# Optimization experiments

Hardware: AMD Instinct MI355X
Metric: run time of the kernel (lower is better)

Reference implementation:

```python
import jax, jax.numpy as jnp
import numpy as np
from jax import lax

C = 128
N_HEADS = 4
HEAD_D = C // N_HEADS
EXP = 2  # FFN expansion


def _ln_c(x, g, b, eps):
    # LayerNorm over channel dim of NCHW (equivalent to to_3d -> LN(c) -> to_4d)
    m = jnp.mean(x, axis=1, keepdims=True)
    v = jnp.mean((x - m) ** 2, axis=1, keepdims=True)
    return (x - m) / jnp.sqrt(v + eps) * g[None, :, None, None] + b[None, :, None, None]


def _conv1x1(x, w, b):
    # w: (out, in)
    return jnp.einsum('bchw,oc->bohw', x, w) + b[None, :, None, None]


def _dwconv(x, w, b):
    # depthwise conv, w: (Cg, 1, k, k), stride 1, SAME padding
    y = lax.conv_general_dilated(
        x, w, window_strides=(1, 1), padding='SAME',
        dimension_numbers=('NCHW', 'OIHW', 'NCHW'),
        feature_group_count=x.shape[1])
    return y + b[None, :, None, None]


def setup_inputs() -> dict:
    key = jax.random.key(0)
    ks = jax.random.split(key, 24)
    s = 0.05
    hid = C
    e = EXP * C
    inp = {
        'feats1': jax.random.normal(ks[0], (2, C, 64, 256), jnp.float32),
        'feats2': jax.random.normal(ks[1], (2, C, 64, 256), jnp.float32),
        # attention norms
        'an_g': jnp.ones((C,), jnp.float32), 'an_b': jnp.zeros((C,), jnp.float32),
        'anc_g': jnp.ones((C,), jnp.float32), 'anc_b': jnp.zeros((C,), jnp.float32),
        # qkv / out 1x1 convs
        'wq': jax.random.normal(ks[2], (hid, C), jnp.float32) * s,
        'bq': jnp.zeros((hid,), jnp.float32),
        'wkv': jax.random.normal(ks[3], (2 * hid, C), jnp.float32) * s,
        'bkv': jnp.zeros((2 * hid,), jnp.float32),
        'wo': jax.random.normal(ks[4], (C, hid), jnp.float32) * s,
        'bo': jnp.zeros((C,), jnp.float32),
        # FFN
        'fn_g': jnp.ones((C,), jnp.float32), 'fn_b': jnp.zeros((C,), jnp.float32),
        'w_in': jax.random.normal(ks[5], (e, C), jnp.float32) * s,
        'b_in': jnp.zeros((e,), jnp.float32),
        'w_dw3': jax.random.normal(ks[6], (e, 1, 3, 3), jnp.float32) * s,
        'b_dw3': jnp.zeros((e,), jnp.float32),
        'w_dw5': jax.random.normal(ks[7], (e, 1, 5, 5), jnp.float32) * s,
        'b_dw5': jnp.zeros((e,), jnp.float32),
        'w_dw7': jax.random.normal(ks[8], (e, 1, 7, 7), jnp.float32) * s,
        'b_dw7': jnp.zeros((e,), jnp.float32),
        'w_pw': jax.random.normal(ks[9], (e, 3 * e), jnp.float32) * s,
        'b_pw': jnp.zeros((e,), jnp.float32),
        'w_out': jax.random.normal(ks[10], (C, e), jnp.float32) * s,
        'b_out': jnp.zeros((C,), jnp.float32),
    }
    return inp


def reference(feats1, feats2, an_g, an_b, anc_g, anc_b, wq, bq, wkv, bkv, wo, bo,
              fn_g, fn_b, w_in, b_in, w_dw3, b_dw3, w_dw5, b_dw5, w_dw7, b_dw7,
              w_pw, b_pw, w_out, b_out):
    eps = 1e-6
    hid = C
    n, d = N_HEADS, HEAD_D
    scale = d ** (-0.5)

    # bi-directional cross attention: doubled batch
    cat1 = jnp.concatenate([feats1, feats2], axis=0)  # (B, C, H, W)
    cat2 = jnp.concatenate([feats2, feats1], axis=0)
    B, _, H, W = cat1.shape

    # pre-norm (separate norms for query and context streams)
    x1 = _ln_c(cat1, an_g, an_b, eps)
    x2 = _ln_c(cat2, anc_g, anc_b, eps)

    q = _conv1x1(x1, wq, bq)                     # (B, hid, H, W)
    kv = _conv1x1(x2, wkv, bkv)
    k, v = kv[:, :hid], kv[:, hid:]

    qh = q.reshape(B, n, d, H, W)
    kh = k.reshape(B, n, d, H, W)
    vh = v.reshape(B, n, d, H, W)

    # per-row (epipolar) attention over width
    sim = jnp.einsum('bndhi,bndhj->bnhij', qh, kh) * scale  # (B, n, H, W, W)
    # sink competition renorm
    attn = jax.nn.softmax(sim, axis=-1) + eps
    attn = attn / jnp.sum(attn, axis=-1, keepdims=True)

    o = jnp.einsum('bnhij,bndhj->bndhi', attn, vh).reshape(B, hid, H, W)
    o = _conv1x1(o, wo, bo)
    cat1 = cat1 + o

    # multiscale depthwise-conv FFN (receptive_aug='conv')
    y = _ln_c(cat1, fn_g, fn_b, 1e-5)
    y = jax.nn.silu(_conv1x1(y, w_in, b_in))     # (B, 2C, H, W)
    f3 = _dwconv(y, w_dw3, b_dw3)
    f5 = _dwconv(y, w_dw5, b_dw5)
    f7 = _dwconv(y, w_dw7, b_dw7)
    y = y + jax.nn.silu(_conv1x1(jnp.concatenate([f3, f5, f7], axis=1), w_pw, b_pw))
    y = _conv1x1(y, w_out, b_out)
    cat1 = cat1 + y

    half = B // 2
    return cat1[:half], cat1[half:]
```

## Files before the change

### kernel.cpp

```cpp
#include <hip/hip_runtime.h>

typedef unsigned short u16;
typedef unsigned int u32;

constexpr int H_ = 64;
constexpr int W_ = 256;
constexpr int HW_ = H_ * W_;

typedef __bf16 bf16x8 __attribute__((ext_vector_type(8)));
typedef float f32x4 __attribute__((ext_vector_type(4)));

__device__ __forceinline__ float bf2f(u16 v) { return __uint_as_float(((u32)v) << 16); }
__device__ __forceinline__ u16 f2bf(float f) {
  u32 x = __float_as_uint(f);
  u32 r = (x + 0x7fffu + ((x >> 16) & 1u)) >> 16;
  return (u16)r;
}
__device__ __forceinline__ float lo2f(u32 p) { return __uint_as_float(p << 16); }
__device__ __forceinline__ float hi2f(u32 p) { return __uint_as_float(p & 0xffff0000u); }
__device__ __forceinline__ void unpack8(uint4 v, float* f) {
  f[0] = lo2f(v.x); f[1] = hi2f(v.x);
  f[2] = lo2f(v.y); f[3] = hi2f(v.y);
  f[4] = lo2f(v.z); f[5] = hi2f(v.z);
  f[6] = lo2f(v.w); f[7] = hi2f(v.w);
}
__device__ __forceinline__ bf16x8 as_bf16x8(uint4 v) {
  union { uint4 u; bf16x8 b; } x; x.u = v; return x.b;
}
__device__ __forceinline__ int swz(int p, int c) { return c ^ (((p >> 3) & 3) << 3); }

constexpr int NT = 26;
constexpr int ELEMS_PER_BLK = 4096;
struct CvtArgs {
  const void* src[NT];
  u32 dst_off[NT];
  u32 n[NT];
  u32 blk_start[NT];
};

__global__ void convert_all(CvtArgs a, u16* __restrict__ dst) {
  const u32 bid = blockIdx.x;
  int ti = 0;
#pragma unroll
  for (int k = 1; k < NT; ++k) if (a.blk_start[k] <= bid) ti = k;
  const u32 e0 = (bid - a.blk_start[ti]) * ELEMS_PER_BLK;
  const u32 n = a.n[ti];
  u32 hi = e0 + ELEMS_PER_BLK; if (hi > n) hi = n;
  const float* sp = (const float*)a.src[ti];
  u16* d = dst + a.dst_off[ti];
  for (u32 i = e0 + threadIdx.x; i < hi; i += 256) d[i] = f2bf(sp[i]);
}

template <int CIN, int COUT>
__launch_bounds__(256)
__global__ void gemm1x1_ln(const u16* __restrict__ xA, const u16* __restrict__ xB,
                           const u16* __restrict__ w, const u16* __restrict__ bias,
                           const u16* __restrict__ lng, const u16* __restrict__ lnb,
                           float lneps, u16* __restrict__ out) {
  constexpr int POS = 64;
  constexpr int PITCH = CIN + 8;
  constexpr int MT = COUT / 64;
  __shared__ __align__(16) u16 xs[POS * PITCH];
  __shared__ float red1[256], red2[256], stm[64], str[64];
  const int t = threadIdx.x;
  const int b = blockIdx.y;
  const int pos0 = blockIdx.x * POS;

  const u16* basep = (b >= 2) ? xB : xA;
  const int bb = (b < 2) ? b : b - 2;
  const u16* xb16 = basep + (size_t)bb * CIN * HW_;

  constexpr int NLOAD = CIN * POS / 8;
  for (int idx = t; idx < NLOAD; idx += 256) {
    const int c = idx / (POS / 8);
    const int p8 = (idx % (POS / 8)) * 8;
    uint4 v = *(const uint4*)(xb16 + (size_t)c * HW_ + pos0 + p8);
    const int csw = swz(p8, c);
    u16* row = xs + p8 * PITCH + csw;
    row[0]         = (u16)v.x; row[PITCH]     = (u16)(v.x >> 16);
    row[2 * PITCH] = (u16)v.y; row[3 * PITCH] = (u16)(v.y >> 16);
    row[4 * PITCH] = (u16)v.z; row[5 * PITCH] = (u16)(v.z >> 16);
    row[6 * PITCH] = (u16)v.w; row[7 * PITCH] = (u16)(v.w >> 16);
  }
  __syncthreads();

  {
    const int p = t & 63, part = t >> 6;
    const int xorp = ((p >> 3) & 3) << 3;
    float s = 0.f, sq = 0.f;
#pragma unroll
    for (int k = 0; k < 32; k += 8) {
      uint4 v = *(const uint4*)(xs + p * PITCH + ((part * 32 + k) ^ xorp));
      float f[8]; unpack8(v, f);
#pragma unroll
      for (int j = 0; j < 8; ++j) { s += f[j]; sq += f[j] * f[j]; }
    }
    red1[part * 64 + p] = s; red2[part * 64 + p] = sq;
    __syncthreads();
    if (t < 64) {
      float ss = red1[t] + red1[64 + t] + red1[128 + t] + red1[192 + t];
      float qq = red2[t] + red2[64 + t] + red2[128 + t] + red2[192 + t];
      float m = ss * (1.0f / CIN);
      float var = qq * (1.0f / CIN) - m * m;
      var = var < 0.f ? 0.f : var;
      stm[t] = m; str[t] = rsqrtf(var + lneps);
    }
    __syncthreads();
    const float m = stm[p], r = str[p];
#pragma unroll
    for (int k = 0; k < 32; k += 8) {
      const int c = part * 32 + k;
      uint4 v = *(const uint4*)(xs + p * PITCH + (c ^ xorp));
      float f[8]; unpack8(v, f);
      u32 pk[4];
#pragma unroll
      for (int j = 0; j < 8; j += 2) {
        float g0 = bf2f(lng[c + j]), be0 = bf2f(lnb[c + j]);
        float g1 = bf2f(lng[c + j + 1]), be1 = bf2f(lnb[c + j + 1]);
        u16 lo = f2bf((f[j] - m) * r * g0 + be0);
        u16 hi = f2bf((f[j + 1] - m) * r * g1 + be1);
        pk[j >> 1] = (u32)lo | ((u32)hi << 16);
      }
      uint4 ov; ov.x = pk[0]; ov.y = pk[1]; ov.z = pk[2]; ov.w = pk[3];
      *(uint4*)(xs + p * PITCH + (c ^ xorp)) = ov;
    }
    __syncthreads();
  }

  const int lane = t & 63, wv = t >> 6;
  const int lo16 = lane & 15, quad = lane >> 4;
  const int orow0 = wv * MT * 16;
  const int qrow = quad * 4;

  f32x4 acc[MT][4];
#pragma unroll
  for (int mt = 0; mt < MT; ++mt) {
#pragma unroll
    for (int r = 0; r < 4; ++r) {
      const float bv = bf2f(bias[orow0 + mt * 16 + qrow + r]);
#pragma unroll
      for (int nt = 0; nt < 4; ++nt) acc[mt][nt][r] = bv;
    }
  }

  const u16* xb[4];
#pragma unroll
  for (int nt = 0; nt < 4; ++nt) {
    const int row = nt * 16 + lo16;
    xb[nt] = xs + row * PITCH + (quad * 8 ^ ((((row >> 3) & 3)) << 3));
  }
  const u16* wl = w + (size_t)(orow0 + lo16) * CIN + quad * 8;

#pragma unroll 2
  for (int kc = 0; kc < CIN / 32; ++kc) {
    const int c0 = kc * 32;
    bf16x8 bfr[4];
#pragma unroll
    for (int nt = 0; nt < 4; ++nt)
      bfr[nt] = as_bf16x8(*(const uint4*)(xb[nt] + c0));
#pragma unroll
    for (int mt = 0; mt < MT; ++mt) {
      bf16x8 afr = as_bf16x8(*(const uint4*)(wl + (size_t)mt * 16 * CIN + c0));
#pragma unroll
      for (int nt = 0; nt < 4; ++nt)
        acc[mt][nt] = __builtin_amdgcn_mfma_f32_16x16x32_bf16(afr, bfr[nt], acc[mt][nt], 0, 0, 0);
    }
  }

#pragma unroll
  for (int mt = 0; mt < MT; ++mt) {
#pragma unroll
    for (int nt = 0; nt < 4; ++nt) {
#pragma unroll
      for (int r = 0; r < 4; ++r) {
        const int o = orow0 + mt * 16 + qrow + r;
        const int p = pos0 + nt * 16 + lo16;
        out[((size_t)b * COUT + o) * HW_ + p] = f2bf(acc[mt][nt][r]);
      }
    }
  }
}

__launch_bounds__(256)
__global__ void attn_mfma(const u16* __restrict__ qb, const u16* __restrict__ kvb,
                          u16* __restrict__ ob) {
  constexpr int PA = 40;
  constexpr int PJ = 264;
  __shared__ __align__(16) u16 kT[256 * PA];
  __shared__ __align__(16) u16 vT[32 * PJ];
  __shared__ __align__(16) u16 PlO[4 * 16 * PJ];
  const int t = threadIdx.x;
  const int h = blockIdx.x, n = blockIdx.y, b = blockIdx.z;
  const size_t qbase = ((size_t)(b * 128 + n * 32)) * HW_ + (size_t)h * W_;
  const size_t kbase = ((size_t)(b * 256 + n * 32)) * HW_ + (size_t)h * W_;
  const size_t vbase = ((size_t)(b * 256 + 128 + n * 32)) * HW_ + (size_t)h * W_;

#pragma unroll
  for (int d8 = 0; d8 < 4; ++d8) {
    u32 pk[4];
#pragma unroll
    for (int j = 0; j < 4; ++j) {
      u32 lo = kvb[kbase + (size_t)(d8 * 8 + 2 * j) * HW_ + t];
      u32 hi = kvb[kbase + (size_t)(d8 * 8 + 2 * j + 1) * HW_ + t];
      pk[j] = lo | (hi << 16);
    }
    *(uint4*)(kT + t * PA + d8 * 8) = make_uint4(pk[0], pk[1], pk[2], pk[3]);
  }
#pragma unroll
  for (int k = 0; k < 16; ++k) {
    const int idx = k * 256 + t;
    const int d = idx >> 7, p2 = (idx & 127) * 2;
    u32 v = *(const u32*)(kvb + vbase + (size_t)d * HW_ + p2);
    *(u32*)(vT + d * PJ + p2) = v;
  }
  __syncthreads();

  const int lane = t & 63, wv = t >> 6;
  const int lo16 = lane & 15, quad = lane >> 4;
  const float scale = 0.17677669529663687f;
  const float renorm = 1.0f / (1.0f + 256.0f * 1e-6f);
  const float addc = 1e-6f * renorm;
  u16* Pw = PlO + wv * 16 * PJ;

  f32x4 oacc[4][2];
  for (int ii = 0; ii < 4; ++ii) {
    const int i0 = ii * 64 + wv * 16;
    u16 qr[8];
#pragma unroll
    for (int j = 0; j < 8; ++j)
      qr[j] = qb[qbase + (size_t)(quad * 8 + j) * HW_ + i0 + lo16];
    bf16x8 qa;
#pragma unroll
    for (int j = 0; j < 8; ++j) qa[j] = *(__bf16*)&qr[j];
    f32x4 s[16];
#pragma unroll
    for (int jt = 0; jt < 16; ++jt) {
      bf16x8 kb = as_bf16x8(*(const uint4*)(kT + (jt * 16 + lo16) * PA + quad * 8));
      f32x4 z = {0.f, 0.f, 0.f, 0.f};
      s[jt] = __builtin_amdgcn_mfma_f32_16x16x32_bf16(qa, kb, z, 0, 0, 0);
    }
#pragma unroll
    for (int r = 0; r < 4; ++r) {
      float sum = 0.f;
#pragma unroll
      for (int jt = 0; jt < 16; ++jt) {
        float e = __expf(s[jt][r] * scale);
        s[jt][r] = e; sum += e;
      }
#pragma unroll
      for (int off = 1; off <= 8; off <<= 1) sum += __shfl_xor(sum, off, 64);
      const float inv2 = renorm / sum;
#pragma unroll
      for (int jt = 0; jt < 16; ++jt)
        Pw[(quad * 4 + r) * PJ + jt * 16 + lo16] = f2bf(fmaf(s[jt][r], inv2, addc));
    }
    f32x4 o0 = {0.f, 0.f, 0.f, 0.f}, o1 = {0.f, 0.f, 0.f, 0.f};
#pragma unroll
    for (int kt = 0; kt < 8; ++kt) {
      bf16x8 pa = as_bf16x8(*(const uint4*)(Pw + lo16 * PJ + kt * 32 + quad * 8));
      bf16x8 v0 = as_bf16x8(*(const uint4*)(vT + lo16 * PJ + kt * 32 + quad * 8));
      bf16x8 v1 = as_bf16x8(*(const uint4*)(vT + (16 + lo16) * PJ + kt * 32 + quad * 8));
      o0 = __builtin_amdgcn_mfma_f32_16x16x32_bf16(pa, v0, o0, 0, 0, 0);
      o1 = __builtin_amdgcn_mfma_f32_16x16x32_bf16(pa, v1, o1, 0, 0, 0);
    }
    oacc[ii][0] = o0; oacc[ii][1] = o1;
  }
  __syncthreads();
  u16* Ob = PlO;
#pragma unroll
  for (int ii = 0; ii < 4; ++ii) {
    const int i0 = ii * 64 + wv * 16;
#pragma unroll
    for (int r = 0; r < 4; ++r) {
      Ob[(i0 + quad * 4 + r) * PA + lo16] = f2bf(oacc[ii][0][r]);
      Ob[(i0 + quad * 4 + r) * PA + 16 + lo16] = f2bf(oacc[ii][1][r]);
    }
  }
  __syncthreads();
  for (int d = 0; d < 32; ++d) ob[qbase + (size_t)d * HW_ + t] = Ob[t * PA + d];
}

__launch_bounds__(256)
__global__ void fused_proj_ffn(const u16* __restrict__ obf,
                               const u16* __restrict__ wo, const u16* __restrict__ bo_,
                               const float* __restrict__ f1, const float* __restrict__ f2,
                               const u16* __restrict__ fng, const u16* __restrict__ fnb,
                               const u16* __restrict__ w_in, const u16* __restrict__ b_in,
                               u16* __restrict__ cat1b, u16* __restrict__ yb) {
  constexpr int PITCH = 136;
  __shared__ __align__(16) u16 xs[64 * PITCH];
  __shared__ float red1[256], red2[256], stm[64], str[64];
  const int t = threadIdx.x;
  const int b = blockIdx.y;
  const int pos0 = blockIdx.x * 64;
  const u16* xb16 = obf + (size_t)b * 128 * HW_;

  for (int idx = t; idx < 1024; idx += 256) {
    const int c = idx >> 3, p8 = (idx & 7) * 8;
    uint4 v = *(const uint4*)(xb16 + (size_t)c * HW_ + pos0 + p8);
    const int csw = swz(p8, c);
    u16* row = xs + p8 * PITCH + csw;
    row[0]         = (u16)v.x; row[PITCH]     = (u16)(v.x >> 16);
    row[2 * PITCH] = (u16)v.y; row[3 * PITCH] = (u16)(v.y >> 16);
    row[4 * PITCH] = (u16)v.z; row[5 * PITCH] = (u16)(v.z >> 16);
    row[6 * PITCH] = (u16)v.w; row[7 * PITCH] = (u16)(v.w >> 16);
  }
  __syncthreads();

  const int lane = t & 63, wv = t >> 6;
  const int lo16 = lane & 15, quad = lane >> 4, qrow = quad * 4;
  const u16* xb[4];
#pragma unroll
  for (int nt = 0; nt < 4; ++nt) {
    const int row = nt * 16 + lo16;
    xb[nt] = xs + row * PITCH + (quad * 8 ^ ((((row >> 3) & 3)) << 3));
  }

  const int orow0 = wv * 32;
  f32x4 acc1[2][4];
#pragma unroll
  for (int mt = 0; mt < 2; ++mt)
#pragma unroll
    for (int r = 0; r < 4; ++r) {
      const float bv = bf2f(bo_[orow0 + mt * 16 + qrow + r]);
#pragma unroll
      for (int nt = 0; nt < 4; ++nt) acc1[mt][nt][r] = bv;
    }
  const u16* wl1 = wo + (size_t)(orow0 + lo16) * 128 + quad * 8;
#pragma unroll
  for (int kc = 0; kc < 4; ++kc) {
    const int c0 = kc * 32;
    bf16x8 bfr[4];
#pragma unroll
    for (int nt = 0; nt < 4; ++nt) bfr[nt] = as_bf16x8(*(const uint4*)(xb[nt] + c0));
#pragma unroll
    for (int mt = 0; mt < 2; ++mt) {
      bf16x8 afr = as_bf16x8(*(const uint4*)(wl1 + (size_t)mt * 16 * 128 + c0));
#pragma unroll
      for (int nt = 0; nt < 4; ++nt)
        acc1[mt][nt] = __builtin_amdgcn_mfma_f32_16x16x32_bf16(afr, bfr[nt], acc1[mt][nt], 0, 0, 0);
    }
  }
  __syncthreads();

  {
    const int bl = (b < 2) ? b : b - 2;
    const float* rb = (b < 2) ? f1 : f2;
#pragma unroll
    for (int mt = 0; mt < 2; ++mt)
#pragma unroll
      for (int nt = 0; nt < 4; ++nt)
#pragma unroll
        for (int r = 0; r < 4; ++r) {
          const int o = orow0 + mt * 16 + qrow + r;
          const int p = nt * 16 + lo16;
          float v = acc1[mt][nt][r] + rb[((size_t)bl * 128 + o) * HW_ + pos0 + p];
          const u16 bv = f2bf(v);
          cat1b[((size_t)b * 128 + o) * HW_ + pos0 + p] = bv;
          xs[p * PITCH + swz(p, o)] = bv;
        }
  }
  __syncthreads();

  {
    const int p = t & 63, part = t >> 6;
    const int xorp = ((p >> 3) & 3) << 3;
    float s = 0.f, sq = 0.f;
#pragma unroll
    for (int k = 0; k < 32; k += 8) {
      uint4 v = *(const uint4*)(xs + p * PITCH + ((part * 32 + k) ^ xorp));
      float f[8]; unpack8(v, f);
#pragma unroll
      for (int j = 0; j < 8; ++j) { s += f[j]; sq += f[j] * f[j]; }
    }
    red1[part * 64 + p] = s; red2[part * 64 + p] = sq;
    __syncthreads();
    if (t < 64) {
      float ss = red1[t] + red1[64 + t] + red1[128 + t] + red1[192 + t];
      float qq = red2[t] + red2[64 + t] + red2[128 + t] + red2[192 + t];
      float m = ss * (1.0f / 128.0f);
      float var = qq * (1.0f / 128.0f) - m * m;
      var = var < 0.f ? 0.f : var;
      stm[t] = m; str[t] = rsqrtf(var + 1e-5f);
    }
    __syncthreads();
    const float m = stm[p], r = str[p];
#pragma unroll
    for (int k = 0; k < 32; k += 8) {
      const int c = part * 32 + k;
      uint4 v = *(const uint4*)(xs + p * PITCH + (c ^ xorp));
      float f[8]; unpack8(v, f);
      u32 pk[4];
#pragma unroll
      for (int j = 0; j < 8; j += 2) {
        float g0 = bf2f(fng[c + j]), be0 = bf2f(fnb[c + j]);
        float g1 = bf2f(fng[c + j + 1]), be1 = bf2f(fnb[c + j + 1]);
        u16 lo = f2bf((f[j] - m) * r * g0 + be0);
        u16 hi = f2bf((f[j + 1] - m) * r * g1 + be1);
        pk[j >> 1] = (u32)lo | ((u32)hi << 16);
      }
      uint4 ov; ov.x = pk[0]; ov.y = pk[1]; ov.z = pk[2]; ov.w = pk[3];
      *(uint4*)(xs + p * PITCH + (c ^ xorp)) = ov;
    }
    __syncthreads();
  }

  const int orow2 = wv * 64;
  f32x4 acc2[4][4];
#pragma unroll
  for (int mt = 0; mt < 4; ++mt)
#pragma unroll
    for (int r = 0; r < 4; ++r) {
      const float bv = bf2f(b_in[orow2 + mt * 16 + qrow + r]);
#pragma unroll
      for (int nt = 0; nt < 4; ++nt) acc2[mt][nt][r] = bv;
    }
  const u16* wl2 = w_in + (size_t)(orow2 + lo16) * 128 + quad * 8;
#pragma unroll
  for (int kc = 0; kc < 4; ++kc) {
    const int c0 = kc * 32;
    bf16x8 bfr[4];
#pragma unroll
    for (int nt = 0; nt < 4; ++nt) bfr[nt] = as_bf16x8(*(const uint4*)(xb[nt] + c0));
#pragma unroll
    for (int mt = 0; mt < 4; ++mt) {
      bf16x8 afr = as_bf16x8(*(const uint4*)(wl2 + (size_t)mt * 16 * 128 + c0));
#pragma unroll
      for (int nt = 0; nt < 4; ++nt)
        acc2[mt][nt] = __builtin_amdgcn_mfma_f32_16x16x32_bf16(afr, bfr[nt], acc2[mt][nt], 0, 0, 0);
    }
  }
#pragma unroll
  for (int mt = 0; mt < 4; ++mt)
#pragma unroll
    for (int nt = 0; nt < 4; ++nt)
#pragma unroll
      for (int r = 0; r < 4; ++r) {
        const int o = orow2 + mt * 16 + qrow + r;
        const int p = nt * 16 + lo16;
        float v = acc2[mt][nt][r];
        v = v / (1.0f + __expf(-v));
        yb[((size_t)b * 256 + o) * HW_ + pos0 + p] = f2bf(v);
      }
}

__launch_bounds__(512, 4)
__global__ void fused_pw_out(const u16* __restrict__ fbase, size_t f_stride,
                             const u16* __restrict__ w_pw, const u16* __restrict__ b_pw,
                             const u16* __restrict__ yb,
                             const u16* __restrict__ w_out, const u16* __restrict__ b_out,
                             const u16* __restrict__ cat1b, float* __restrict__ outp,
                             int b_off) {
  constexpr int SP = 136;
  constexpr int P2 = 264;
  constexpr int NCHK = 6;
  __shared__ __align__(16) u16 sbuf[2][64 * SP];
  u16* y2 = &sbuf[0][0];

  const int t = threadIdx.x;
  const int bo2 = (int)blockIdx.y + b_off;
  const int pos0 = blockIdx.x * 64;
  const u16* xf = fbase + (size_t)blockIdx.y * f_stride;

  const int lane = t & 63, wv = t >> 6;
  const int lo16 = lane & 15, quad = lane >> 4, qrow = quad * 4;

  const int c_s0 = t >> 3;
  const int c_s1 = c_s0 + 64;
  const int p8_s = (t & 7) * 8;
  const size_t g_off = pos0 + p8_s;

  uint4 pf0, pf1;
  pf0 = *(const uint4*)(xf + (size_t)c_s0 * HW_ + g_off);
  pf1 = *(const uint4*)(xf + (size_t)c_s1 * HW_ + g_off);
  {
    u16* r0 = sbuf[0] + p8_s * SP + swz(p8_s, c_s0);
    r0[0]      = (u16)pf0.x; r0[SP]     = (u16)(pf0.x >> 16);
    r0[2 * SP] = (u16)pf0.y; r0[3 * SP] = (u16)(pf0.y >> 16);
    r0[4 * SP] = (u16)pf0.z; r0[5 * SP] = (u16)(pf0.z >> 16);
    r0[6 * SP] = (u16)pf0.w; r0[7 * SP] = (u16)(pf0.w >> 16);
    u16* r1 = sbuf[0] + p8_s * SP + swz(p8_s, c_s1);
    r1[0]      = (u16)pf1.x; r1[SP]     = (u16)(pf1.x >> 16);
    r1[2 * SP] = (u16)pf1.y; r1[3 * SP] = (u16)(pf1.y >> 16);
    r1[4 * SP] = (u16)pf1.z; r1[5 * SP] = (u16)(pf1.z >> 16);
    r1[6 * SP] = (u16)pf1.w; r1[7 * SP] = (u16)(pf1.w >> 16);
  }
  pf0 = *(const uint4*)(xf + (size_t)(128 + c_s0) * HW_ + g_off);
  pf1 = *(const uint4*)(xf + (size_t)(128 + c_s1) * HW_ + g_off);

  const int orow1 = wv * 32;
  f32x4 acc[2][4];
#pragma unroll
  for (int mt = 0; mt < 2; ++mt)
#pragma unroll
    for (int r = 0; r < 4; ++r) {
      const float bv = bf2f(b_pw[orow1 + mt * 16 + qrow + r]);
#pragma unroll
      for (int nt = 0; nt < 4; ++nt) acc[mt][nt][r] = bv;
    }
  int xoff[4];
#pragma unroll
  for (int nt = 0; nt < 4; ++nt) {
    const int row = nt * 16 + lo16;
    xoff[nt] = row * SP + (quad * 8 ^ ((((row >> 3) & 3)) << 3));
  }
  const u16* wl1 = w_pw + (size_t)(orow1 + lo16) * 768 + quad * 8;

  __syncthreads();

  for (int ch = 0; ch < NCHK; ++ch) {
    if (ch + 1 < NCHK) {
      u16* dst = sbuf[(ch + 1) & 1];
      u16* r0 = dst + p8_s * SP + swz(p8_s, c_s0);
      r0[0]      = (u16)pf0.x; r0[SP]     = (u16)(pf0.x >> 16);
      r0[2 * SP] = (u16)pf0.y; r0[3 * SP] = (u16)(pf0.y >> 16);
      r0[4 * SP] = (u16)pf0.z; r0[5 * SP] = (u16)(pf0.z >> 16);
      r0[6 * SP] = (u16)pf0.w; r0[7 * SP] = (u16)(pf0.w >> 16);
      u16* r1 = dst + p8_s * SP + swz(p8_s, c_s1);
      r1[0]      = (u16)pf1.x; r1[SP]     = (u16)(pf1.x >> 16);
      r1[2 * SP] = (u16)pf1.y; r1[3 * SP] = (u16)(pf1.y >> 16);
      r1[4 * SP] = (u16)pf1.z; r1[5 * SP] = (u16)(pf1.z >> 16);
      r1[6 * SP] = (u16)pf1.w; r1[7 * SP] = (u16)(pf1.w >> 16);
    }
    if (ch + 2 < NCHK) {
      pf0 = *(const uint4*)(xf + (size_t)((ch + 2) * 128 + c_s0) * HW_ + g_off);
      pf1 = *(const uint4*)(xf + (size_t)((ch + 2) * 128 + c_s1) * HW_ + g_off);
    }
    const u16* xs = sbuf[ch & 1];
    const u16* wch = wl1 + ch * 128;
#pragma unroll
    for (int kc = 0; kc < 4; ++kc) {
      const int c0 = kc * 32;
      bf16x8 bfr[4];
#pragma unroll
      for (int nt = 0; nt < 4; ++nt)
        bfr[nt] = as_bf16x8(*(const uint4*)(xs + xoff[nt] + c0));
#pragma unroll
      for (int mt = 0; mt < 2; ++mt) {
        bf16x8 afr = as_bf16x8(*(const uint4*)(wch + (size_t)mt * 16 * 768 + c0));
#pragma unroll
        for (int nt = 0; nt < 4; ++nt)
          acc[mt][nt] = __builtin_amdgcn_mfma_f32_16x16x32_bf16(afr, bfr[nt], acc[mt][nt], 0, 0, 0);
      }
    }
    __syncthreads();
  }

#pragma unroll
  for (int mt = 0; mt < 2; ++mt)
#pragma unroll
    for (int nt = 0; nt < 4; ++nt)
#pragma unroll
      for (int r = 0; r < 4; ++r) {
        const int o = orow1 + mt * 16 + qrow + r;
        const int p = nt * 16 + lo16;
        float v = acc[mt][nt][r];
        v = v / (1.0f + __expf(-v));
        v += bf2f(yb[((size_t)bo2 * 256 + o) * HW_ + pos0 + p]);
        y2[p * P2 + swz(p, o)] = f2bf(v);
      }
  __syncthreads();

  int x2off[4];
#pragma unroll
  for (int nt = 0; nt < 4; ++nt) {
    const int row = nt * 16 + lo16;
    x2off[nt] = row * P2 + (quad * 8 ^ ((((row >> 3) & 3)) << 3));
  }
  const int orow2 = wv * 16;
  f32x4 acc2[4];
#pragma unroll
  for (int r = 0; r < 4; ++r) {
    const float bv = bf2f(b_out[orow2 + qrow + r]);
#pragma unroll
    for (int nt = 0; nt < 4; ++nt) acc2[nt][r] = bv;
  }
  const u16* wl2 = w_out + (size_t)(orow2 + lo16) * 256 + quad * 8;
#pragma unroll
  for (int kc = 0; kc < 8; ++kc) {
    const int c0 = kc * 32;
    bf16x8 bfr[4];
#pragma unroll
    for (int nt = 0; nt < 4; ++nt) bfr[nt] = as_bf16x8(*(const uint4*)(y2 + x2off[nt] + c0));
    bf16x8 afr = as_bf16x8(*(const uint4*)(wl2 + c0));
#pragma unroll
    for (int nt = 0; nt < 4; ++nt)
      acc2[nt] = __builtin_amdgcn_mfma_f32_16x16x32_bf16(afr, bfr[nt], acc2[nt], 0, 0, 0);
  }
#pragma unroll
  for (int nt = 0; nt < 4; ++nt)
#pragma unroll
    for (int r = 0; r < 4; ++r) {
      const int o = orow2 + qrow + r;
      const int p = nt * 16 + lo16;
      const size_t gidx = ((size_t)bo2 * 128 + o) * HW_ + pos0 + p;
      outp[gidx] = acc2[nt][r] + bf2f(cat1b[gidx]);
    }
}

__launch_bounds__(256)
__global__ void dwconv_kernel(const u16* __restrict__ yB,
                              const u16* __restrict__ w3, const u16* __restrict__ b3,
                              const u16* __restrict__ w5, const u16* __restrict__ b5,
                              const u16* __restrict__ w7, const u16* __restrict__ b7,
                              u16* __restrict__ fB) {
  constexpr int TP = 272;
  __shared__ __align__(16) float tile[10 * TP];
  __shared__ __align__(16) float wf7p[56];
  __shared__ __align__(16) float wf5p[40];
  __shared__ __align__(16) float wf3p[12];
  const int t = threadIdx.x;
  const int c = blockIdx.y;
  const int bz = blockIdx.z;
  const int h0 = blockIdx.x * 4;
  const u16* src = yB + ((size_t)bz * 256 + c) * HW_;

  if (t < 56) {
    const int rr = t >> 3, dx = t & 7;
    wf7p[t] = (dx < 7) ? bf2f(w7[c * 49 + rr * 7 + dx]) : 0.f;
  } else if (t >= 64 && t < 104) {
    const int i = t - 64, rr = i >> 3, dx = i & 7;
    wf5p[i] = (dx < 5) ? bf2f(w5[c * 25 + rr * 5 + dx]) : 0.f;
  } else if (t >= 112 && t < 124) {
    const int i = t - 112, rr = i >> 2, dx = i & 3;
    wf3p[i] = (dx < 3) ? bf2f(w3[c * 9 + rr * 3 + dx]) : 0.f;
  }

  for (int idx = t; idx < 10 * 132; idx += 256) {
    const int r = idx / 132, cx = idx - r * 132;
    const int gh = h0 + r - 3, gw = cx * 2 - 4;
    float v0 = 0.f, v1 = 0.f;
    if (gh >= 0 && gh < H_ && gw >= 0 && gw < W_ - 1) {
      const u32 v = *(const u32*)(src + gh * W_ + gw);
      v0 = lo2f(v); v1 = hi2f(v);
    }
    tile[r * TP + 2 * cx] = v0;
    tile[r * TP + 2 * cx + 1] = v1;
  }
  __syncthreads();

  const int hh = t >> 6;
  const int x0 = (t & 63) * 4;
  float a3[4], a5[4], a7[4];
#pragma unroll
  for (int j = 0; j < 4; ++j) { a3[j] = 0.f; a5[j] = 0.f; a7[j] = 0.f; }

#pragma unroll 1
  for (int rr = 0; rr < 7; ++rr) {
    const float* tr = tile + (hh + rr) * TP + x0;
    f32x4 v0 = *(const f32x4*)(tr);
    f32x4 v1 = *(const f32x4*)(tr + 4);
    f32x4 v2 = *(const f32x4*)(tr + 8);
    float g[12] = {v0[0], v0[1], v0[2], v0[3], v1[0], v1[1], v1[2], v1[3],
                   v2[0], v2[1], v2[2], v2[3]};
    {
      f32x4 wa = *(const f32x4*)(wf7p + rr * 8);
      f32x4 wb = *(const f32x4*)(wf7p + rr * 8 + 4);
#pragma unroll
      for (int p = 0; p < 4; ++p) {
        float s = a7[p];
        s = fmaf(wa[0], g[p + 1], s);
        s = fmaf(wa[1], g[p + 2], s);
        s = fmaf(wa[2], g[p + 3], s);
        s = fmaf(wa[3], g[p + 4], s);
        s = fmaf(wb[0], g[p + 5], s);
        s = fmaf(wb[1], g[p + 6], s);
        s = fmaf(wb[2], g[p + 7], s);
        a7[p] = s;
      }
    }
    if (rr >= 1 && rr <= 5) {
      f32x4 wa = *(const f32x4*)(wf5p + (rr - 1) * 8);
      const float w4v = wf5p[(rr - 1) * 8 + 4];
#pragma unroll
      for (int p = 0; p < 4; ++p) {
        float s = a5[p];
        s = fmaf(wa[0], g[p + 2], s);
        s = fmaf(wa[1], g[p + 3], s);
        s = fmaf(wa[2], g[p + 4], s);
        s = fmaf(wa[3], g[p + 5], s);
        s = fmaf(w4v, g[p + 6], s);
        a5[p] = s;
      }
    }
    if (rr >= 2 && rr <= 4) {
      f32x4 wv = *(const f32x4*)(wf3p + (rr - 2) * 4);
#pragma unroll
      for (int p = 0; p < 4; ++p) {
        float s = a3[p];
        s = fmaf(wv[0], g[p + 3], s);
        s = fmaf(wv[1], g[p + 4], s);
        s = fmaf(wv[2], g[p + 5], s);
        a3[p] = s;
      }
    }
  }

  const float B3v = bf2f(b3[c]), B5v = bf2f(b5[c]), B7v = bf2f(b7[c]);
  uint2 o3, o5, o7;
  o3.x = (u32)f2bf(a3[0] + B3v) | ((u32)f2bf(a3[1] + B3v) << 16);
  o3.y = (u32)f2bf(a3[2] + B3v) | ((u32)f2bf(a3[3] + B3v) << 16);
  o5.x = (u32)f2bf(a5[0] + B5v) | ((u32)f2bf(a5[1] + B5v) << 16);
  o5.y = (u32)f2bf(a5[2] + B5v) | ((u32)f2bf(a5[3] + B5v) << 16);
  o7.x = (u32)f2bf(a7[0] + B7v) | ((u32)f2bf(a7[1] + B7v) << 16);
  o7.y = (u32)f2bf(a7[2] + B7v) | ((u32)f2bf(a7[3] + B7v) << 16);
  const size_t o0 = (size_t)bz * 768 * HW_ + (size_t)c * HW_ + (size_t)(h0 + hh) * W_ + x0;
  *(uint2*)(fB + o0) = o3;
  *(uint2*)(fB + o0 + (size_t)256 * HW_) = o5;
  *(uint2*)(fB + o0 + (size_t)512 * HW_) = o7;
}

extern "C" void kernel_launch(void* const* d_in, const int* in_sizes, int n_in,
                              void* d_out, int out_size, void* d_ws, size_t ws_size,
                              hipStream_t stream) {
  (void)out_size; (void)n_in;
  char* ws = (char*)d_ws;
  const size_t MB = 1ull << 20;

  u16* arena = (u16*)ws;
  CvtArgs ca;
  u32 off = 0, blk = 0;
  u32 aoff[NT];
  for (int i = 0; i < NT; ++i) {
    ca.src[i] = d_in[i];
    ca.n[i] = (u32)in_sizes[i];
    ca.dst_off[i] = off;
    aoff[i] = off;
    ca.blk_start[i] = blk;
    off += (ca.n[i] + 15u) & ~15u;
    blk += (ca.n[i] + ELEMS_PER_BLK - 1) / ELEMS_PER_BLK;
  }
  const u32 total_blocks = blk;

  const u16* f1c   = arena + aoff[0];
  const u16* f2c   = arena + aoff[1];
  const u16* an_g  = arena + aoff[2];
  const u16* an_b  = arena + aoff[3];
  const u16* anc_g = arena + aoff[4];
  const u16* anc_b = arena + aoff[5];
  const u16* wq    = arena + aoff[6];
  const u16* bq    = arena + aoff[7];
  const u16* wkv   = arena + aoff[8];
  const u16* bkv   = arena + aoff[9];
  const u16* wo    = arena + aoff[10];
  const u16* bo_   = arena + aoff[11];
  const u16* fn_g  = arena + aoff[12];
  const u16* fn_b  = arena + aoff[13];
  const u16* w_in  = arena + aoff[14];
  const u16* b_in  = arena + aoff[15];
  const u16* w3    = arena + aoff[16];
  const u16* b3    = arena + aoff[17];
  const u16* w5    = arena + aoff[18];
  const u16* b5    = arena + aoff[19];
  const u16* w7    = arena + aoff[20];
  const u16* b7    = arena + aoff[21];
  const u16* w_pw  = arena + aoff[22];
  const u16* b_pw  = arena + aoff[23];
  const u16* w_out = arena + aoff[24];
  const u16* b_out = arena + aoff[25];

  u16* cat1b  = (u16*)(ws + 18 * MB);
  u16* qb     = (u16*)(ws + 34 * MB);
  u16* kvb    = (u16*)(ws + 50 * MB);
  u16* obf    = (u16*)(ws + 82 * MB);
  u16* yb     = (u16*)(ws + 34 * MB);
  u16* fbuf   = (u16*)(ws + 66 * MB);
  float* outp = (float*)d_out;
  const bool big = ws_size >= 168 * MB;

  dim3 blk256(256);
  dim3 blk512(512);
  convert_all<<<total_blocks, 256, 0, stream>>>(ca, arena);

  gemm1x1_ln<128, 128><<<dim3(HW_ / 64, 4), blk256, 0, stream>>>(
      f1c, f2c, wq, bq, an_g, an_b, 1e-6f, qb);
  gemm1x1_ln<128, 256><<<dim3(HW_ / 64, 4), blk256, 0, stream>>>(
      f2c, f1c, wkv, bkv, anc_g, anc_b, 1e-6f, kvb);
  attn_mfma<<<dim3(64, 4, 4), blk256, 0, stream>>>(qb, kvb, obf);
  fused_proj_ffn<<<dim3(HW_ / 64, 4), blk256, 0, stream>>>(
      obf, wo, bo_, (const float*)d_in[0], (const float*)d_in[1],
      fn_g, fn_b, w_in, b_in, cat1b, yb);
  if (big) {
    dwconv_kernel<<<dim3(16, 256, 4), blk256, 0, stream>>>(yb, w3, b3, w5, b5, w7, b7, fbuf);
    fused_pw_out<<<dim3(HW_ / 64, 4), blk512, 0, stream>>>(
        fbuf, (size_t)768 * HW_, w_pw, b_pw, yb, w_out, b_out, cat1b, outp, 0);
  } else {
    for (int b = 0; b < 4; ++b) {
      dwconv_kernel<<<dim3(16, 256, 1), blk256, 0, stream>>>(
          yb + (size_t)b * 256 * HW_, w3, b3, w5, b5, w7, b7, fbuf);
      fused_pw_out<<<dim3(HW_ / 64, 1), blk512, 0, stream>>>(
          fbuf, 0, w_pw, b_pw, yb, w_out, b_out, cat1b, outp, b);
    }
  }
}
```

Before: 364.8 us.

## Retile fused_pw_out to 32-pixel tiles with 256 threads and packed LDS stores

The fused pointwise+output GEMM kernel moves from 64-pixel tiles with 512 threads to 32-pixel tiles with 256 threads. Each wave now covers 64 output rows instead of 32, so every B fragment read from LDS feeds more MFMAs. The grid has twice as many blocks. The staging store is rewritten to pack two channels into one 32-bit LDS write, with a new XOR swizzle applied at 32-element granularity. The risk is that each weight fragment is now reused over fewer pixels, weights get loaded more times in total, and per-thread register pressure goes up.

```diff
diff --git a/kernel.cpp b/kernel.cpp
--- a/kernel.cpp
+++ b/kernel.cpp
@@ -444,7 +444,7 @@
       }
 }
 
-__launch_bounds__(512, 4)
+__launch_bounds__(256)
 __global__ void fused_pw_out(const u16* __restrict__ fbase, size_t f_stride,
                              const u16* __restrict__ w_pw, const u16* __restrict__ b_pw,
                              const u16* __restrict__ yb,
@@ -454,55 +454,56 @@
   constexpr int SP = 136;
   constexpr int P2 = 264;
   constexpr int NCHK = 6;
-  __shared__ __align__(16) u16 sbuf[2][64 * SP];
+  __shared__ __align__(16) u16 sbuf[2][32 * SP];
   u16* y2 = &sbuf[0][0];
 
   const int t = threadIdx.x;
   const int bo2 = (int)blockIdx.y + b_off;
-  const int pos0 = blockIdx.x * 64;
+  const int pos0 = blockIdx.x * 32;
   const u16* xf = fbase + (size_t)blockIdx.y * f_stride;
 
   const int lane = t & 63, wv = t >> 6;
   const int lo16 = lane & 15, quad = lane >> 4, qrow = quad * 4;
 
-  const int c_s0 = t >> 3;
-  const int c_s1 = c_s0 + 64;
-  const int p8_s = (t & 7) * 8;
+  const int e = t >> 2;
+  const int m = t & 3;
+  const int p8_s = m * 8;
   const size_t g_off = pos0 + p8_s;
+  const int wbase = p8_s * SP + ((2 * e) ^ (m << 5));
 
   uint4 pf0, pf1;
-  pf0 = *(const uint4*)(xf + (size_t)c_s0 * HW_ + g_off);
-  pf1 = *(const uint4*)(xf + (size_t)c_s1 * HW_ + g_off);
+  pf0 = *(const uint4*)(xf + (size_t)(2 * e) * HW_ + g_off);
+  pf1 = *(const uint4*)(xf + (size_t)(2 * e + 1) * HW_ + g_off);
   {
-    u16* r0 = sbuf[0] + p8_s * SP + swz(p8_s, c_s0);
-    r0[0]      = (u16)pf0.x; r0[SP]     = (u16)(pf0.x >> 16);
-    r0[2 * SP] = (u16)pf0.y; r0[3 * SP] = (u16)(pf0.y >> 16);
-    r0[4 * SP] = (u16)pf0.z; r0[5 * SP] = (u16)(pf0.z >> 16);
-    r0[6 * SP] = (u16)pf0.w; r0[7 * SP] = (u16)(pf0.w >> 16);
-    u16* r1 = sbuf[0] + p8_s * SP + swz(p8_s, c_s1);
-    r1[0]      = (u16)pf1.x; r1[SP]     = (u16)(pf1.x >> 16);
-    r1[2 * SP] = (u16)pf1.y; r1[3 * SP] = (u16)(pf1.y >> 16);
-    r1[4 * SP] = (u16)pf1.z; r1[5 * SP] = (u16)(pf1.z >> 16);
-    r1[6 * SP] = (u16)pf1.w; r1[7 * SP] = (u16)(pf1.w >> 16);
-  }
-  pf0 = *(const uint4*)(xf + (size_t)(128 + c_s0) * HW_ + g_off);
-  pf1 = *(const uint4*)(xf + (size_t)(128 + c_s1) * HW_ + g_off);
-
-  const int orow1 = wv * 32;
-  f32x4 acc[2][4];
-#pragma unroll
-  for (int mt = 0; mt < 2; ++mt)
+    u16* d = sbuf[0] + wbase;
+    *(u32*)(d)          = (pf0.x & 0xffffu) | (pf1.x << 16);
+    *(u32*)(d + SP)     = (pf0.x >> 16) | (pf1.x & 0xffff0000u);
+    *(u32*)(d + 2 * SP) = (pf0.y & 0xffffu) | (pf1.y << 16);
+    *(u32*)(d + 3 * SP) = (pf0.y >> 16) | (pf1.y & 0xffff0000u);
+    *(u32*)(d + 4 * SP) = (pf0.z & 0xffffu) | (pf1.z << 16);
+    *(u32*)(d + 5 * SP) = (pf0.z >> 16) | (pf1.z & 0xffff0000u);
+    *(u32*)(d + 6 * SP) = (pf0.w & 0xffffu) | (pf1.w << 16);
+    *(u32*)(d + 7 * SP) = (pf0.w >> 16) | (pf1.w & 0xffff0000u);
+  }
+  pf0 = *(const uint4*)(xf + (size_t)(128 + 2 * e) * HW_ + g_off);
+  pf1 = *(const uint4*)(xf + (size_t)(128 + 2 * e + 1) * HW_ + g_off);
+
+  const int orow1 = wv * 64;
+  f32x4 acc[4][2];
+#pragma unroll
+  for (int mt = 0; mt < 4; ++mt)
 #pragma unroll
     for (int r = 0; r < 4; ++r) {
       const float bv = bf2f(b_pw[orow1 + mt * 16 + qrow + r]);
 #pragma unroll
-      for (int nt = 0; nt < 4; ++nt) acc[mt][nt][r] = bv;
-    }
-  int xoff[4];
-#pragma unroll
-  for (int nt = 0; nt < 4; ++nt) {
+      for (int nt = 0; nt < 2; ++nt) acc[mt][nt][r] = bv;
+    }
+  int xrow[2], xorr[2];
+#pragma unroll
+  for (int nt = 0; nt < 2; ++nt) {
     const int row = nt * 16 + lo16;
-    xoff[nt] = row * SP + (quad * 8 ^ ((((row >> 3) & 3)) << 3));
+    xrow[nt] = row * SP + quad * 8;
+    xorr[nt] = ((row >> 3) & 3) << 5;
   }
   const u16* wl1 = w_pw + (size_t)(orow1 + lo16) * 768 + quad * 8;
 
@@ -510,36 +511,34 @@
 
   for (int ch = 0; ch < NCHK; ++ch) {
     if (ch + 1 < NCHK) {
-      u16* dst = sbuf[(ch + 1) & 1];
-      u16* r0 = dst + p8_s * SP + swz(p8_s, c_s0);
-      r0[0]      = (u16)pf0.x; r0[SP]     = (u16)(pf0.x >> 16);
-      r0[2 * SP] = (u16)pf0.y; r0[3 * SP] = (u16)(pf0.y >> 16);
-      r0[4 * SP] = (u16)pf0.z; r0[5 * SP] = (u16)(pf0.z >> 16);
-      r0[6 * SP] = (u16)pf0.w; r0[7 * SP] = (u16)(pf0.w >> 16);
-      u16* r1 = dst + p8_s * SP + swz(p8_s, c_s1);
-      r1[0]      = (u16)pf1.x; r1[SP]     = (u16)(pf1.x >> 16);
-      r1[2 * SP] = (u16)pf1.y; r1[3 * SP] = (u16)(pf1.y >> 16);
-      r1[4 * SP] = (u16)pf1.z; r1[5 * SP] = (u16)(pf1.z >> 16);
-      r1[6 * SP] = (u16)pf1.w; r1[7 * SP] = (u16)(pf1.w >> 16);
+      u16* d = sbuf[(ch + 1) & 1] + wbase;
+      *(u32*)(d)          = (pf0.x & 0xffffu) | (pf1.x << 16);
+      *(u32*)(d + SP)     = (pf0.x >> 16) | (pf1.x & 0xffff0000u);
+      *(u32*)(d + 2 * SP) = (pf0.y & 0xffffu) | (pf1.y << 16);
+      *(u32*)(d + 3 * SP) = (pf0.y >> 16) | (pf1.y & 0xffff0000u);
+      *(u32*)(d + 4 * SP) = (pf0.z & 0xffffu) | (pf1.z << 16);
+      *(u32*)(d + 5 * SP) = (pf0.z >> 16) | (pf1.z & 0xffff0000u);
+      *(u32*)(d + 6 * SP) = (pf0.w & 0xffffu) | (pf1.w << 16);
+      *(u32*)(d + 7 * SP) = (pf0.w >> 16) | (pf1.w & 0xffff0000u);
     }
     if (ch + 2 < NCHK) {
-      pf0 = *(const uint4*)(xf + (size_t)((ch + 2) * 128 + c_s0) * HW_ + g_off);
-      pf1 = *(const uint4*)(xf + (size_t)((ch + 2) * 128 + c_s1) * HW_ + g_off);
+      pf0 = *(const uint4*)(xf + (size_t)((ch + 2) * 128 + 2 * e) * HW_ + g_off);
+      pf1 = *(const uint4*)(xf + (size_t)((ch + 2) * 128 + 2 * e + 1) * HW_ + g_off);
     }
     const u16* xs = sbuf[ch & 1];
     const u16* wch = wl1 + ch * 128;
 #pragma unroll
     for (int kc = 0; kc < 4; ++kc) {
       const int c0 = kc * 32;
-      bf16x8 bfr[4];
-#pragma unroll
-      for (int nt = 0; nt < 4; ++nt)
-        bfr[nt] = as_bf16x8(*(const uint4*)(xs + xoff[nt] + c0));
-#pragma unroll
-      for (int mt = 0; mt < 2; ++mt) {
+      bf16x8 bfr[2];
+#pragma unroll
+      for (int nt = 0; nt < 2; ++nt)
+        bfr[nt] = as_bf16x8(*(const uint4*)(xs + xrow[nt] + (c0 ^ xorr[nt])));
+#pragma unroll
+      for (int mt = 0; mt < 4; ++mt) {
         bf16x8 afr = as_bf16x8(*(const uint4*)(wch + (size_t)mt * 16 * 768 + c0));
 #pragma unroll
-        for (int nt = 0; nt < 4; ++nt)
+        for (int nt = 0; nt < 2; ++nt)
           acc[mt][nt] = __builtin_amdgcn_mfma_f32_16x16x32_bf16(afr, bfr[nt], acc[mt][nt], 0, 0, 0);
       }
     }
@@ -547,9 +546,9 @@
   }
 
 #pragma unroll
-  for (int mt = 0; mt < 2; ++mt)
-#pragma unroll
-    for (int nt = 0; nt < 4; ++nt)
+  for (int mt = 0; mt < 4; ++mt)
+#pragma unroll
+    for (int nt = 0; nt < 2; ++nt)
 #pragma unroll
       for (int r = 0; r < 4; ++r) {
         const int o = orow1 + mt * 16 + qrow + r;
@@ -557,45 +556,54 @@
         float v = acc[mt][nt][r];
         v = v / (1.0f + __expf(-v));
         v += bf2f(yb[((size_t)bo2 * 256 + o) * HW_ + pos0 + p]);
-        y2[p * P2 + swz(p, o)] = f2bf(v);
-      }
-  __syncthreads();
-
-  int x2off[4];
-#pragma unroll
-  for (int nt = 0; nt < 4; ++nt) {
+        y2[p * P2 + (o ^ (((p >> 3) & 3) << 5))] = f2bf(v);
+      }
+  __syncthreads();
+
+  int x2row[2], x2or[2];
+#pragma unroll
+  for (int nt = 0; nt < 2; ++nt) {
     const int row = nt * 16 + lo16;
-    x2off[nt] = row * P2 + (quad * 8 ^ ((((row >> 3) & 3)) << 3));
-  }
-  const int orow2 = wv * 16;
-  f32x4 acc2[4];
-#pragma unroll
-  for (int r = 0; r < 4; ++r) {
-    const float bv = bf2f(b_out[orow2 + qrow + r]);
-#pragma unroll
-    for (int nt = 0; nt < 4; ++nt) acc2[nt][r] = bv;
-  }
+    x2row[nt] = row * P2 + quad * 8;
+    x2or[nt] = ((row >> 3) & 3) << 5;
+  }
+  const int orow2 = wv * 32;
+  f32x4 acc2[2][2];
+#pragma unroll
+  for (int mt = 0; mt < 2; ++mt)
+#pragma unroll
+    for (int r = 0; r < 4; ++r) {
+      const float bv = bf2f(b_out[orow2 + mt * 16 + qrow + r]);
+#pragma unroll
+      for (int nt = 0; nt < 2; ++nt) acc2[mt][nt][r] = bv;
+    }
   const u16* wl2 = w_out + (size_t)(orow2 + lo16) * 256 + quad * 8;
 #pragma unroll
   for (int kc = 0; kc < 8; ++kc) {
     const int c0 = kc * 32;
-    bf16x8 bfr[4];
-#pragma unroll
-    for (int nt = 0; nt < 4; ++nt) bfr[nt] = as_bf16x8(*(const uint4*)(y2 + x2off[nt] + c0));
-    bf16x8 afr = as_bf16x8(*(const uint4*)(wl2 + c0));
-#pragma unroll
-    for (int nt = 0; nt < 4; ++nt)
-      acc2[nt] = __builtin_amdgcn_mfma_f32_16x16x32_bf16(afr, bfr[nt], acc2[nt], 0, 0, 0);
-  }
-#pragma unroll
-  for (int nt = 0; nt < 4; ++nt)
-#pragma unroll
-    for (int r = 0; r < 4; ++r) {
-      const int o = orow2 + qrow + r;
-      const int p = nt * 16 + lo16;
-      const size_t gidx = ((size_t)bo2 * 128 + o) * HW_ + pos0 + p;
-      outp[gidx] = acc2[nt][r] + bf2f(cat1b[gidx]);
-    }
+    bf16x8 bfr[2];
+#pragma unroll
+    for (int nt = 0; nt < 2; ++nt)
+      bfr[nt] = as_bf16x8(*(const uint4*)(y2 + x2row[nt] + (c0 ^ x2or[nt])));
+#pragma unroll
+    for (int mt = 0; mt < 2; ++mt) {
+      bf16x8 afr = as_bf16x8(*(const uint4*)(wl2 + (size_t)mt * 16 * 256 + c0));
+#pragma unroll
+      for (int nt = 0; nt < 2; ++nt)
+        acc2[mt][nt] = __builtin_amdgcn_mfma_f32_16x16x32_bf16(afr, bfr[nt], acc2[mt][nt], 0, 0, 0);
+    }
+  }
+#pragma unroll
+  for (int mt = 0; mt < 2; ++mt)
+#pragma unroll
+    for (int nt = 0; nt < 2; ++nt)
+#pragma unroll
+      for (int r = 0; r < 4; ++r) {
+        const int o = orow2 + mt * 16 + qrow + r;
+        const int p = nt * 16 + lo16;
+        const size_t gidx = ((size_t)bo2 * 128 + o) * HW_ + pos0 + p;
+        outp[gidx] = acc2[mt][nt][r] + bf2f(cat1b[gidx]);
+      }
 }
 
 __launch_bounds__(256)
@@ -769,7 +777,6 @@
   const bool big = ws_size >= 168 * MB;
 
   dim3 blk256(256);
-  dim3 blk512(512);
   convert_all<<<total_blocks, 256, 0, stream>>>(ca, arena);
 
   gemm1x1_ln<128, 128><<<dim3(HW_ / 64, 4), blk256, 0, stream>>>(
@@ -782,13 +789,13 @@
       fn_g, fn_b, w_in, b_in, cat1b, yb);
   if (big) {
     dwconv_kernel<<<dim3(16, 256, 4), blk256, 0, stream>>>(yb, w3, b3, w5, b5, w7, b7, fbuf);
-    fused_pw_out<<<dim3(HW_ / 64, 4), blk512, 0, stream>>>(
+    fused_pw_out<<<dim3(HW_ / 32, 4), blk256, 0, stream>>>(
         fbuf, (size_t)768 * HW_, w_pw, b_pw, yb, w_out, b_out, cat1b, outp, 0);
   } else {
     for (int b = 0; b < 4; ++b) {
       dwconv_kernel<<<dim3(16, 256, 1), blk256, 0, stream>>>(
           yb + (size_t)b * 256 * HW_, w3, b3, w5, b5, w7, b7, fbuf);
-      fused_pw_out<<<dim3(HW_ / 64, 1), blk512, 0, stream>>>(
+      fused_pw_out<<<dim3(HW_ / 32, 1), blk256, 0, stream>>>(
           fbuf, 0, w_pw, b_pw, yb, w_out, b_out, cat1b, outp, b);
     }
   }
```

Result: slower. 420.3 us (+15.2%).
